# Performance work log

Hardware: AMD Instinct MI355X
Metric: run time of the kernel (lower is better)

The kernel has to match this reference:

```python
import jax, jax.numpy as jnp
import numpy as np

B, S, HID = 1, 2048, 4096
NH, NKV = 32, 8
HD = HID // NH          # 128
N_REP = NH // NKV       # 4
ROPE_THETA = 10000.0


def setup_inputs() -> dict:
    key = jax.random.key(0)
    ks = jax.random.split(key, 5)
    scale = 0.02
    x = jax.random.normal(ks[0], (B, S, HID), dtype=jnp.float32)
    Wq = jax.random.normal(ks[1], (HID, HID), dtype=jnp.float32) * scale
    Wk = jax.random.normal(ks[2], (NKV * HD, HID), dtype=jnp.float32) * scale
    Wv = jax.random.normal(ks[3], (NKV * HD, HID), dtype=jnp.float32) * scale
    Wo = jax.random.normal(ks[4], (HID, HID), dtype=jnp.float32) * scale
    position_ids = jnp.broadcast_to(jnp.arange(S, dtype=jnp.int32)[None, :], (B, S))
    return {"x": x, "Wq": Wq, "Wk": Wk, "Wv": Wv, "Wo": Wo, "position_ids": position_ids}


def _rope_cache(seq_len, dtype):
    inv_freq = 1.0 / (ROPE_THETA ** (jnp.arange(0, HD, 2, dtype=jnp.float32) / HD))
    t = jnp.arange(seq_len, dtype=jnp.float32)
    freqs = t[:, None] * inv_freq[None, :]            # [S, HD/2]
    emb = jnp.concatenate([freqs, freqs], axis=-1)    # [S, HD]
    return jnp.cos(emb).astype(dtype), jnp.sin(emb).astype(dtype)


def _rotate_half(x):
    x1, x2 = x[..., : HD // 2], x[..., HD // 2:]
    return jnp.concatenate([-x2, x1], axis=-1)


def reference(x, Wq, Wk, Wv, Wo, position_ids):
    b, s, _ = x.shape
    # projections (nn.Linear: x @ W.T)
    q = (x @ Wq.T).reshape(b, s, NH, HD).transpose(0, 2, 1, 3)    # [B,NH,S,HD]
    k = (x @ Wk.T).reshape(b, s, NKV, HD).transpose(0, 2, 1, 3)   # [B,NKV,S,HD]
    v = (x @ Wv.T).reshape(b, s, NKV, HD).transpose(0, 2, 1, 3)
    # RoPE
    cos_c, sin_c = _rope_cache(s, x.dtype)
    cos = cos_c[position_ids][:, None, :, :]   # [B,1,S,HD]
    sin = sin_c[position_ids][:, None, :, :]
    q = q * cos + _rotate_half(q) * sin
    k = k * cos + _rotate_half(k) * sin
    # GQA repeat_kv
    k = jnp.repeat(k, N_REP, axis=1)   # [B,NH,S,HD]
    v = jnp.repeat(v, N_REP, axis=1)
    # scaled dot-product attention with causal mask
    scores = jnp.einsum('bhqd,bhkd->bhqk', q, k) / jnp.sqrt(jnp.float32(HD))
    causal = jnp.tril(jnp.ones((s, s), dtype=bool))
    scores = jnp.where(causal[None, None, :, :], scores, jnp.finfo(scores.dtype).min)
    attn = jax.nn.softmax(scores.astype(jnp.float32), axis=-1).astype(q.dtype)
    out = jnp.einsum('bhqk,bhkd->bhqd', attn, v)                  # [B,NH,S,HD]
    out = out.transpose(0, 2, 1, 3).reshape(b, s, NH * HD)
    return out @ Wo.T
```

## Files before the change

kernel.cpp:

```cpp
#include <hip/hip_runtime.h>
#include <hip/hip_bf16.h>

#define DEVI __device__ __forceinline__

typedef __attribute__((ext_vector_type(8))) __bf16 bf16x8;
typedef __attribute__((ext_vector_type(4))) float f32x4;

DEVI f32x4 mfma_16x16x32(bf16x8 a, bf16x8 b, f32x4 c) {
  return __builtin_amdgcn_mfma_f32_16x16x32_bf16(a, b, c, 0, 0, 0);
}

DEVI void gld16(const void* g, void* l) {
  __builtin_amdgcn_global_load_lds(
      reinterpret_cast<const __attribute__((address_space(1))) unsigned int*>(
          reinterpret_cast<unsigned long long>(g)),
      reinterpret_cast<__attribute__((address_space(3))) unsigned int*>(
          reinterpret_cast<unsigned long long>(l)),
      16, 0, 0);
}

DEVI unsigned short f2bf(float f) {
  unsigned u = __builtin_bit_cast(unsigned, f);
  u += 0x7FFFu + ((u >> 16) & 1u);
  return (unsigned short)(u >> 16);
}
DEVI float bf2f(unsigned short b) {
  return __builtin_bit_cast(float, (unsigned)b << 16);
}

struct Conv5 {
  const float4 *x, *wq, *wk, *wv, *wo;
  ushort4 *xb, *wqb, *wkv, *wob;
};
__global__ void k_conv_all(Conv5 a) {
  constexpr int C0 = 2097152;
  constexpr int C1 = C0 + 4194304;
  constexpr int C2 = C1 + 1048576;
  constexpr int C3 = C2 + 1048576;
  constexpr int C4 = C3 + 4194304;
  int stride = gridDim.x * blockDim.x;
  for (int i = blockIdx.x * blockDim.x + threadIdx.x; i < C4; i += stride) {
    const float4* src; ushort4* dst; int j;
    if (i < C0)      { src = a.x;  dst = a.xb;            j = i; }
    else if (i < C1) { src = a.wq; dst = a.wqb;           j = i - C0; }
    else if (i < C2) { src = a.wk; dst = a.wkv;           j = i - C1; }
    else if (i < C3) { src = a.wv; dst = a.wkv + 1048576; j = i - C2; }
    else             { src = a.wo; dst = a.wob;           j = i - C3; }
    float4 v = src[j];
    ushort4 o; o.x = f2bf(v.x); o.y = f2bf(v.y); o.z = f2bf(v.z); o.w = f2bf(v.w);
    dst[j] = o;
  }
}

__global__ void k_rope_table(float2* __restrict__ tab) {
  int idx = blockIdx.x * blockDim.x + threadIdx.x;
  int s = idx >> 6, d = idx & 63;
  float invf = powf(10000.0f, -(float)d * (1.0f / 64.0f));
  float f = (float)s * invf;
  tab[idx] = make_float2(cosf(f), sinf(f));
}

template <int NH_, int L2NH>
__global__ void k_rope_v(unsigned short* __restrict__ X, const float2* __restrict__ tab,
                         const int* __restrict__ pos, float scale) {
  int t = blockIdx.x * blockDim.x + threadIdx.x;
  int d0 = (t & 7) * 8;
  int sh = t >> 3;
  int s  = sh >> L2NH;
  int h  = sh & (NH_ - 1);
  size_t base = (size_t)s * (NH_ * 128) + h * 128 + d0;
  const float4* tf = (const float4*)(tab + (size_t)pos[s] * 64 + d0);
  unsigned short a[8], b[8], oa[8], ob[8];
  *(ushort4*)&a[0] = *(const ushort4*)(X + base);
  *(ushort4*)&a[4] = *(const ushort4*)(X + base + 4);
  *(ushort4*)&b[0] = *(const ushort4*)(X + base + 64);
  *(ushort4*)&b[4] = *(const ushort4*)(X + base + 68);
#pragma unroll
  for (int j = 0; j < 4; ++j) {
    float4 cs = tf[j];
    float x1 = bf2f(a[2*j]),   x2 = bf2f(b[2*j]);
    float y1 = bf2f(a[2*j+1]), y2 = bf2f(b[2*j+1]);
    oa[2*j]   = f2bf((x1 * cs.x - x2 * cs.y) * scale);
    ob[2*j]   = f2bf((x2 * cs.x + x1 * cs.y) * scale);
    oa[2*j+1] = f2bf((y1 * cs.z - y2 * cs.w) * scale);
    ob[2*j+1] = f2bf((y2 * cs.z + y1 * cs.w) * scale);
  }
  *(ushort4*)(X + base)      = *(ushort4*)&oa[0];
  *(ushort4*)(X + base + 4)  = *(ushort4*)&oa[4];
  *(ushort4*)(X + base + 64) = *(ushort4*)&ob[0];
  *(ushort4*)(X + base + 68) = *(ushort4*)&ob[4];
}

template <int MODE>
__global__ __launch_bounds__(256, 2)
void k_gemm_bt(const unsigned short* __restrict__ A,
               const unsigned short* __restrict__ B,
               void* __restrict__ Cp, int M, int N, int K) {
  constexpr int BK = 32;
  __shared__ __align__(16) unsigned short As[128][BK];
  __shared__ __align__(16) unsigned short Bs[128][BK];
  const int tid  = threadIdx.x;
  const int lane = tid & 63;
  const int wave = tid >> 6;
  const int bm = blockIdx.y * 128;
  const int bn = blockIdx.x * 128;
  const int wm = (wave >> 1) * 64;
  const int wn = (wave & 1) * 64;
  const int l15 = lane & 15;
  const int lg  = lane >> 4;

  f32x4 acc[4][4] = {};

  const int srow = lane >> 2;
  const int scol = (lane & 3) * 8;
  const unsigned short* aS0 = A + (size_t)(bm + wave * 32 + srow) * K + scol;
  const unsigned short* aS1 = aS0 + (size_t)16 * K;
  const unsigned short* bS0 = B + (size_t)(bn + wave * 32 + srow) * K + scol;
  const unsigned short* bS1 = bS0 + (size_t)16 * K;

  for (int k0 = 0; k0 < K; k0 += BK) {
    __syncthreads();
    gld16(aS0 + k0, &As[wave * 32][0]);
    gld16(aS1 + k0, &As[wave * 32 + 16][0]);
    gld16(bS0 + k0, &Bs[wave * 32][0]);
    gld16(bS1 + k0, &Bs[wave * 32 + 16][0]);
    __syncthreads();

    bf16x8 a[4], b[4];
#pragma unroll
    for (int m = 0; m < 4; ++m) a[m] = *(const bf16x8*)&As[wm + m * 16 + l15][lg * 8];
#pragma unroll
    for (int n = 0; n < 4; ++n) b[n] = *(const bf16x8*)&Bs[wn + n * 16 + l15][lg * 8];
#pragma unroll
    for (int m = 0; m < 4; ++m)
#pragma unroll
      for (int n = 0; n < 4; ++n)
        acc[m][n] = mfma_16x16x32(a[m], b[n], acc[m][n]);
  }

#pragma unroll
  for (int m = 0; m < 4; ++m)
#pragma unroll
    for (int n = 0; n < 4; ++n)
#pragma unroll
      for (int r = 0; r < 4; ++r) {
        int row = bm + wm + m * 16 + lg * 4 + r;
        int col = bn + wn + n * 16 + l15;
        float v = acc[m][n][r];
        if (MODE == 0) ((unsigned short*)Cp)[(size_t)row * N + col] = f2bf(v);
        else           ((float*)Cp)[(size_t)row * N + col] = v;
      }
}

__global__ __launch_bounds__(256, 2)
void k_gemm_kv(const unsigned short* __restrict__ A,
               const unsigned short* __restrict__ B,
               unsigned short* __restrict__ Kp,
               unsigned short* __restrict__ Vtp,
               int M, int K) {
  constexpr int BK = 32;
  __shared__ __align__(16) unsigned short As[64][BK];
  __shared__ __align__(16) unsigned short Bs[128][BK];
  const int tid = threadIdx.x, lane = tid & 63, wave = tid >> 6;
  const int bm = blockIdx.y * 64;
  const int bn = blockIdx.x * 128;
  const int wn = wave * 32;
  const int l15 = lane & 15, lg = lane >> 4;
  f32x4 acc[4][2] = {};
  const int srow = lane >> 2, scol = (lane & 3) * 8;
  const unsigned short* aS0 = A + (size_t)(bm + wave * 16 + srow) * K + scol;
  const unsigned short* bS0 = B + (size_t)(bn + wave * 32 + srow) * K + scol;
  const unsigned short* bS1 = bS0 + (size_t)16 * K;

  for (int k0 = 0; k0 < K; k0 += BK) {
    __syncthreads();
    gld16(aS0 + k0, &As[wave * 16][0]);
    gld16(bS0 + k0, &Bs[wave * 32][0]);
    gld16(bS1 + k0, &Bs[wave * 32 + 16][0]);
    __syncthreads();
    bf16x8 a[4], b[2];
#pragma unroll
    for (int m = 0; m < 4; ++m) a[m] = *(const bf16x8*)&As[m * 16 + l15][lg * 8];
#pragma unroll
    for (int n = 0; n < 2; ++n) b[n] = *(const bf16x8*)&Bs[wn + n * 16 + l15][lg * 8];
#pragma unroll
    for (int m = 0; m < 4; ++m)
#pragma unroll
      for (int n = 0; n < 2; ++n)
        acc[m][n] = mfma_16x16x32(a[m], b[n], acc[m][n]);
  }

#pragma unroll
  for (int m = 0; m < 4; ++m)
#pragma unroll
    for (int n = 0; n < 2; ++n)
#pragma unroll
      for (int r = 0; r < 4; ++r) {
        int row = bm + m * 16 + lg * 4 + r;
        int col = bn + wn + n * 16 + l15;
        float v = acc[m][n][r];
        if (col < 1024) Kp[(size_t)row * 1024 + col] = f2bf(v);
        else            Vtp[(size_t)(col - 1024) * 2048 + row] = f2bf(v);
      }
}

__global__ __launch_bounds__(256, 2)
void k_attn(const unsigned short* __restrict__ Q,
            const unsigned short* __restrict__ Kb,
            const unsigned short* __restrict__ Vt,
            unsigned short* __restrict__ AO) {
  __shared__ __align__(16) unsigned short Kl[2][64][128];
  __shared__ __align__(16) unsigned short Vl[2][128][64];
  __shared__ __align__(16) unsigned short Pl[4][16][72];
  const int tid = threadIdx.x, lane = tid & 63, w = tid >> 6;
  const int bid = blockIdx.x;
  const int qi = 31 - (bid >> 5);
  const int h  = bid & 31;
  const int q0 = qi * 64;
  const int kh = h >> 2;
  const int l15 = lane & 15, lg = lane >> 4;

  bf16x8 qf[4];
  {
    const unsigned short* qr = Q + (size_t)(q0 + w * 16 + l15) * 4096 + h * 128;
#pragma unroll
    for (int ks = 0; ks < 4; ++ks) qf[ks] = *(const bf16x8*)(qr + ks * 32 + lg * 8);
  }

  f32x4 o[8] = {};
  float m_run = -1e30f, l_run = 0.f;
  const int nkb = qi + 1;
  const int myq = q0 + w * 16 + l15;

  auto stageK = [&](int buf, int kv0) {
#pragma unroll
    for (int c = 0; c < 4; ++c) {
      int row = 16 * w + 4 * c + lg;
      gld16(Kb + (size_t)(kv0 + row) * 1024 + kh * 128 + ((l15 ^ (row & 7)) * 8),
            &Kl[buf][16 * w + 4 * c][0]);
    }
  };
  auto stageV = [&](int buf, int kv0) {
#pragma unroll
    for (int c = 0; c < 4; ++c) {
      int row = 32 * w + 8 * c + (lane >> 3);
      gld16(Vt + (size_t)(kh * 128 + row) * 2048 + kv0 + (((lane & 7) ^ (row & 7)) * 8),
            &Vl[buf][32 * w + 8 * c][0]);
    }
  };

  stageK(0, 0);
  stageV(0, 0);
  int cur = 0;

  for (int kb = 0; kb < nkb; ++kb) {
    const int kv0 = kb * 64;
    __syncthreads();
    if (kb + 1 < nkb) { stageK(cur ^ 1, kv0 + 64); stageV(cur ^ 1, kv0 + 64); }

    f32x4 s[4] = {};
    __builtin_amdgcn_s_setprio(1);
#pragma unroll
    for (int ks = 0; ks < 4; ++ks)
#pragma unroll
      for (int n = 0; n < 4; ++n) {
        bf16x8 bk = *(const bf16x8*)&Kl[cur][n * 16 + l15][((ks * 4 + lg) ^ (l15 & 7)) * 8];
        s[n] = mfma_16x16x32(bk, qf[ks], s[n]);
      }
    __builtin_amdgcn_s_setprio(0);

    if (kb == nkb - 1) {
#pragma unroll
      for (int n = 0; n < 4; ++n)
#pragma unroll
        for (int r = 0; r < 4; ++r)
          if (kv0 + n * 16 + lg * 4 + r > myq) s[n][r] = -1e30f;
    }

    float mx = -1e30f;
#pragma unroll
    for (int n = 0; n < 4; ++n)
      mx = fmaxf(mx, fmaxf(fmaxf(s[n][0], s[n][1]), fmaxf(s[n][2], s[n][3])));
    mx = fmaxf(mx, __shfl_xor(mx, 16));
    mx = fmaxf(mx, __shfl_xor(mx, 32));
    float mn = fmaxf(m_run, mx);
    float fac = __expf(m_run - mn);
    m_run = mn;
    float rs = 0.f;
#pragma unroll
    for (int n = 0; n < 4; ++n)
#pragma unroll
      for (int r = 0; r < 4; ++r) {
        float pv = __expf(s[n][r] - mn);
        s[n][r] = pv;
        rs += pv;
      }
    rs += __shfl_xor(rs, 16);
    rs += __shfl_xor(rs, 32);
    l_run = l_run * fac + rs;
#pragma unroll
    for (int j = 0; j < 8; ++j) {
      o[j][0] *= fac; o[j][1] *= fac; o[j][2] *= fac; o[j][3] *= fac;
    }

#pragma unroll
    for (int n = 0; n < 4; ++n)
#pragma unroll
      for (int r = 0; r < 4; ++r)
        Pl[w][l15][n * 16 + lg * 4 + r] = f2bf(s[n][r]);
    asm volatile("s_waitcnt lgkmcnt(0)" ::: "memory");
    bf16x8 pa0 = *(const bf16x8*)&Pl[w][l15][lg * 8];
    bf16x8 pa1 = *(const bf16x8*)&Pl[w][l15][32 + lg * 8];

    __builtin_amdgcn_s_setprio(1);
#pragma unroll
    for (int j = 0; j < 8; ++j) {
      bf16x8 bv0 = *(const bf16x8*)&Vl[cur][j * 16 + l15][(lg ^ (l15 & 7)) * 8];
      bf16x8 bv1 = *(const bf16x8*)&Vl[cur][j * 16 + l15][((4 + lg) ^ (l15 & 7)) * 8];
      o[j] = mfma_16x16x32(bv0, pa0, o[j]);
      o[j] = mfma_16x16x32(bv1, pa1, o[j]);
    }
    __builtin_amdgcn_s_setprio(0);
    cur ^= 1;
  }

  float inv = 1.0f / l_run;
  __syncthreads();
  unsigned short* Ol = &Kl[0][0][0];
#pragma unroll
  for (int j = 0; j < 8; ++j)
#pragma unroll
    for (int r = 0; r < 4; ++r)
      Ol[w * 2176 + l15 * 136 + j * 16 + lg * 4 + r] = f2bf(o[j][r] * inv);
  asm volatile("s_waitcnt lgkmcnt(0)" ::: "memory");
#pragma unroll
  for (int p = 0; p < 4; ++p) {
    int row = p * 4 + lg;
    bf16x8 vv = *(const bf16x8*)&Ol[w * 2176 + row * 136 + l15 * 8];
    *(bf16x8*)(AO + (size_t)(q0 + w * 16 + row) * 4096 + h * 128 + l15 * 8) = vv;
  }
}

extern "C" void kernel_launch(void* const* d_in, const int* in_sizes, int n_in,
                              void* d_out, int out_size, void* d_ws, size_t ws_size,
                              hipStream_t stream) {
  const float* x  = (const float*)d_in[0];
  const float* Wq = (const float*)d_in[1];
  const float* Wk = (const float*)d_in[2];
  const float* Wv = (const float*)d_in[3];
  const float* Wo = (const float*)d_in[4];
  const int*   pos = (const int*)d_in[5];
  float* out = (float*)d_out;

  char* p = (char*)d_ws;
  unsigned short* xb  = (unsigned short*)p; p += (size_t)2048 * 4096 * 2;
  unsigned short* wqb = (unsigned short*)p; p += (size_t)4096 * 4096 * 2;
  unsigned short* wkv = (unsigned short*)p; p += (size_t)2048 * 4096 * 2;
  unsigned short* wob = (unsigned short*)p; p += (size_t)4096 * 4096 * 2;
  unsigned short* qb  = (unsigned short*)p; p += (size_t)2048 * 4096 * 2;
  unsigned short* kb  = (unsigned short*)p; p += (size_t)2048 * 1024 * 2;
  unsigned short* vtb = (unsigned short*)p; p += (size_t)1024 * 2048 * 2;
  unsigned short* aob = (unsigned short*)p; p += (size_t)2048 * 4096 * 2;
  float2*         tab = (float2*)p;         p += (size_t)2048 * 64 * 8;

  Conv5 ca;
  ca.x  = (const float4*)x;  ca.wq = (const float4*)Wq; ca.wk = (const float4*)Wk;
  ca.wv = (const float4*)Wv; ca.wo = (const float4*)Wo;
  ca.xb = (ushort4*)xb; ca.wqb = (ushort4*)wqb; ca.wkv = (ushort4*)wkv; ca.wob = (ushort4*)wob;
  k_conv_all<<<4096, 256, 0, stream>>>(ca);
  k_rope_table<<<512, 256, 0, stream>>>(tab);

  k_gemm_bt<0><<<dim3(32, 16), 256, 0, stream>>>(xb, wqb, qb, 2048, 4096, 4096);
  k_gemm_kv<<<dim3(16, 32), 256, 0, stream>>>(xb, wkv, kb, vtb, 2048, 4096);

  const float scale = 0.08838834764831845f;
  k_rope_v<32, 5><<<2048, 256, 0, stream>>>(qb, tab, pos, scale);
  k_rope_v<8, 3><<<512, 256, 0, stream>>>(kb, tab, pos, 1.0f);

  k_attn<<<1024, 256, 0, stream>>>(qb, kb, vtb, aob);

  k_gemm_bt<1><<<dim3(32, 16), 256, 0, stream>>>(aob, wob, out, 2048, 4096, 4096);
}
```

Before: 560.1 us.

## Fuse QKV projections into one GEMM, widen K tile with swizzle, lazy softmax rescale

Packs Wq, Wk and Wv into one contiguous bf16 weight buffer so a single GEMM launch with 48 column tiles produces Q, K and transposed V, and routes each column in the epilogue. The GEMM now loads 64-wide K tiles with an XOR-swizzled LDS layout, halving barrier rounds per K and reducing bank conflicts. The attention kernel skips the running-max rescale unless some row's max grows by more than 8, saving exp and multiplies at some risk to range, and writes P to LDS as packed 4-element stores. LDS per block doubles, which may affect occupancy.

```diff
diff --git a/kernel.cpp b/kernel.cpp
--- a/kernel.cpp
+++ b/kernel.cpp
@@ -30,7 +30,7 @@
 
 struct Conv5 {
   const float4 *x, *wq, *wk, *wv, *wo;
-  ushort4 *xb, *wqb, *wkv, *wob;
+  ushort4 *xb, *wqkv, *wob;
 };
 __global__ void k_conv_all(Conv5 a) {
   constexpr int C0 = 2097152;
@@ -41,11 +41,11 @@
   int stride = gridDim.x * blockDim.x;
   for (int i = blockIdx.x * blockDim.x + threadIdx.x; i < C4; i += stride) {
     const float4* src; ushort4* dst; int j;
-    if (i < C0)      { src = a.x;  dst = a.xb;            j = i; }
-    else if (i < C1) { src = a.wq; dst = a.wqb;           j = i - C0; }
-    else if (i < C2) { src = a.wk; dst = a.wkv;           j = i - C1; }
-    else if (i < C3) { src = a.wv; dst = a.wkv + 1048576; j = i - C2; }
-    else             { src = a.wo; dst = a.wob;           j = i - C3; }
+    if (i < C0)      { src = a.x;  dst = a.xb;             j = i; }
+    else if (i < C1) { src = a.wq; dst = a.wqkv;           j = i - C0; }
+    else if (i < C2) { src = a.wk; dst = a.wqkv + 4194304; j = i - C1; }
+    else if (i < C3) { src = a.wv; dst = a.wqkv + 5242880; j = i - C2; }
+    else             { src = a.wo; dst = a.wob;            j = i - C3; }
     float4 v = src[j];
     ushort4 o; o.x = f2bf(v.x); o.y = f2bf(v.y); o.z = f2bf(v.z); o.w = f2bf(v.w);
     dst[j] = o;
@@ -91,14 +91,16 @@
   *(ushort4*)(X + base + 68) = *(ushort4*)&ob[4];
 }
 
-template <int MODE>
+template <int EPI>
 __global__ __launch_bounds__(256, 2)
-void k_gemm_bt(const unsigned short* __restrict__ A,
-               const unsigned short* __restrict__ B,
-               void* __restrict__ Cp, int M, int N, int K) {
-  constexpr int BK = 32;
-  __shared__ __align__(16) unsigned short As[128][BK];
-  __shared__ __align__(16) unsigned short Bs[128][BK];
+void k_gemm64(const unsigned short* __restrict__ A,
+              const unsigned short* __restrict__ B,
+              void* __restrict__ Cp,
+              unsigned short* __restrict__ Kp,
+              unsigned short* __restrict__ Vtp,
+              int K) {
+  __shared__ __align__(16) unsigned short As[128][64];
+  __shared__ __align__(16) unsigned short Bs[128][64];
   const int tid  = threadIdx.x;
   const int lane = tid & 63;
   const int wave = tid >> 6;
@@ -111,31 +113,35 @@
 
   f32x4 acc[4][4] = {};
 
-  const int srow = lane >> 2;
-  const int scol = (lane & 3) * 8;
-  const unsigned short* aS0 = A + (size_t)(bm + wave * 32 + srow) * K + scol;
-  const unsigned short* aS1 = aS0 + (size_t)16 * K;
-  const unsigned short* bS0 = B + (size_t)(bn + wave * 32 + srow) * K + scol;
-  const unsigned short* bS1 = bS0 + (size_t)16 * K;
-
-  for (int k0 = 0; k0 < K; k0 += BK) {
+  const int srow  = lane >> 3;
+  const int scol  = ((lane & 7) ^ srow) * 8;
+  const unsigned short* aS = A + (size_t)(bm + wave * 32 + srow) * K + scol;
+  const unsigned short* bS = B + (size_t)(bn + wave * 32 + srow) * K + scol;
+
+  for (int k0 = 0; k0 < K; k0 += 64) {
     __syncthreads();
-    gld16(aS0 + k0, &As[wave * 32][0]);
-    gld16(aS1 + k0, &As[wave * 32 + 16][0]);
-    gld16(bS0 + k0, &Bs[wave * 32][0]);
-    gld16(bS1 + k0, &Bs[wave * 32 + 16][0]);
+#pragma unroll
+    for (int c = 0; c < 4; ++c) {
+      gld16(aS + (size_t)(c * 8) * K + k0, &As[wave * 32 + c * 8][0]);
+      gld16(bS + (size_t)(c * 8) * K + k0, &Bs[wave * 32 + c * 8][0]);
+    }
     __syncthreads();
 
-    bf16x8 a[4], b[4];
-#pragma unroll
-    for (int m = 0; m < 4; ++m) a[m] = *(const bf16x8*)&As[wm + m * 16 + l15][lg * 8];
-#pragma unroll
-    for (int n = 0; n < 4; ++n) b[n] = *(const bf16x8*)&Bs[wn + n * 16 + l15][lg * 8];
-#pragma unroll
-    for (int m = 0; m < 4; ++m)
+#pragma unroll
+    for (int ks = 0; ks < 2; ++ks) {
+      bf16x8 a[4], b[4];
+#pragma unroll
+      for (int m = 0; m < 4; ++m)
+        a[m] = *(const bf16x8*)&As[wm + m * 16 + l15][((ks * 4 + lg) ^ (l15 & 7)) * 8];
 #pragma unroll
       for (int n = 0; n < 4; ++n)
-        acc[m][n] = mfma_16x16x32(a[m], b[n], acc[m][n]);
+        b[n] = *(const bf16x8*)&Bs[wn + n * 16 + l15][((ks * 4 + lg) ^ (l15 & 7)) * 8];
+#pragma unroll
+      for (int m = 0; m < 4; ++m)
+#pragma unroll
+        for (int n = 0; n < 4; ++n)
+          acc[m][n] = mfma_16x16x32(a[m], b[n], acc[m][n]);
+    }
   }
 
 #pragma unroll
@@ -147,60 +153,13 @@
         int row = bm + wm + m * 16 + lg * 4 + r;
         int col = bn + wn + n * 16 + l15;
         float v = acc[m][n][r];
-        if (MODE == 0) ((unsigned short*)Cp)[(size_t)row * N + col] = f2bf(v);
-        else           ((float*)Cp)[(size_t)row * N + col] = v;
-      }
-}
-
-__global__ __launch_bounds__(256, 2)
-void k_gemm_kv(const unsigned short* __restrict__ A,
-               const unsigned short* __restrict__ B,
-               unsigned short* __restrict__ Kp,
-               unsigned short* __restrict__ Vtp,
-               int M, int K) {
-  constexpr int BK = 32;
-  __shared__ __align__(16) unsigned short As[64][BK];
-  __shared__ __align__(16) unsigned short Bs[128][BK];
-  const int tid = threadIdx.x, lane = tid & 63, wave = tid >> 6;
-  const int bm = blockIdx.y * 64;
-  const int bn = blockIdx.x * 128;
-  const int wn = wave * 32;
-  const int l15 = lane & 15, lg = lane >> 4;
-  f32x4 acc[4][2] = {};
-  const int srow = lane >> 2, scol = (lane & 3) * 8;
-  const unsigned short* aS0 = A + (size_t)(bm + wave * 16 + srow) * K + scol;
-  const unsigned short* bS0 = B + (size_t)(bn + wave * 32 + srow) * K + scol;
-  const unsigned short* bS1 = bS0 + (size_t)16 * K;
-
-  for (int k0 = 0; k0 < K; k0 += BK) {
-    __syncthreads();
-    gld16(aS0 + k0, &As[wave * 16][0]);
-    gld16(bS0 + k0, &Bs[wave * 32][0]);
-    gld16(bS1 + k0, &Bs[wave * 32 + 16][0]);
-    __syncthreads();
-    bf16x8 a[4], b[2];
-#pragma unroll
-    for (int m = 0; m < 4; ++m) a[m] = *(const bf16x8*)&As[m * 16 + l15][lg * 8];
-#pragma unroll
-    for (int n = 0; n < 2; ++n) b[n] = *(const bf16x8*)&Bs[wn + n * 16 + l15][lg * 8];
-#pragma unroll
-    for (int m = 0; m < 4; ++m)
-#pragma unroll
-      for (int n = 0; n < 2; ++n)
-        acc[m][n] = mfma_16x16x32(a[m], b[n], acc[m][n]);
-  }
-
-#pragma unroll
-  for (int m = 0; m < 4; ++m)
-#pragma unroll
-    for (int n = 0; n < 2; ++n)
-#pragma unroll
-      for (int r = 0; r < 4; ++r) {
-        int row = bm + m * 16 + lg * 4 + r;
-        int col = bn + wn + n * 16 + l15;
-        float v = acc[m][n][r];
-        if (col < 1024) Kp[(size_t)row * 1024 + col] = f2bf(v);
-        else            Vtp[(size_t)(col - 1024) * 2048 + row] = f2bf(v);
+        if (EPI == 0) {
+          if (col < 4096)      ((unsigned short*)Cp)[(size_t)row * 4096 + col] = f2bf(v);
+          else if (col < 5120) Kp[(size_t)row * 1024 + (col - 4096)] = f2bf(v);
+          else                 Vtp[(size_t)(col - 5120) * 2048 + row] = f2bf(v);
+        } else {
+          ((float*)Cp)[(size_t)row * 4096 + col] = v;
+        }
       }
 }
 
@@ -283,31 +242,36 @@
       mx = fmaxf(mx, fmaxf(fmaxf(s[n][0], s[n][1]), fmaxf(s[n][2], s[n][3])));
     mx = fmaxf(mx, __shfl_xor(mx, 16));
     mx = fmaxf(mx, __shfl_xor(mx, 32));
-    float mn = fmaxf(m_run, mx);
-    float fac = __expf(m_run - mn);
-    m_run = mn;
+
+    if (!__all(mx <= m_run + 8.0f)) {
+      float mn = fmaxf(m_run, mx);
+      float fac = __expf(m_run - mn);
+      m_run = mn;
+      l_run *= fac;
+#pragma unroll
+      for (int j = 0; j < 8; ++j) {
+        o[j][0] *= fac; o[j][1] *= fac; o[j][2] *= fac; o[j][3] *= fac;
+      }
+    }
     float rs = 0.f;
 #pragma unroll
     for (int n = 0; n < 4; ++n)
 #pragma unroll
       for (int r = 0; r < 4; ++r) {
-        float pv = __expf(s[n][r] - mn);
+        float pv = __expf(s[n][r] - m_run);
         s[n][r] = pv;
         rs += pv;
       }
     rs += __shfl_xor(rs, 16);
     rs += __shfl_xor(rs, 32);
-    l_run = l_run * fac + rs;
-#pragma unroll
-    for (int j = 0; j < 8; ++j) {
-      o[j][0] *= fac; o[j][1] *= fac; o[j][2] *= fac; o[j][3] *= fac;
-    }
-
-#pragma unroll
-    for (int n = 0; n < 4; ++n)
-#pragma unroll
-      for (int r = 0; r < 4; ++r)
-        Pl[w][l15][n * 16 + lg * 4 + r] = f2bf(s[n][r]);
+    l_run += rs;
+
+#pragma unroll
+    for (int n = 0; n < 4; ++n) {
+      ushort4 pk;
+      pk.x = f2bf(s[n][0]); pk.y = f2bf(s[n][1]); pk.z = f2bf(s[n][2]); pk.w = f2bf(s[n][3]);
+      *(ushort4*)&Pl[w][l15][n * 16 + lg * 4] = pk;
+    }
     asm volatile("s_waitcnt lgkmcnt(0)" ::: "memory");
     bf16x8 pa0 = *(const bf16x8*)&Pl[w][l15][lg * 8];
     bf16x8 pa1 = *(const bf16x8*)&Pl[w][l15][32 + lg * 8];
@@ -353,25 +317,23 @@
   float* out = (float*)d_out;
 
   char* p = (char*)d_ws;
-  unsigned short* xb  = (unsigned short*)p; p += (size_t)2048 * 4096 * 2;
-  unsigned short* wqb = (unsigned short*)p; p += (size_t)4096 * 4096 * 2;
-  unsigned short* wkv = (unsigned short*)p; p += (size_t)2048 * 4096 * 2;
-  unsigned short* wob = (unsigned short*)p; p += (size_t)4096 * 4096 * 2;
-  unsigned short* qb  = (unsigned short*)p; p += (size_t)2048 * 4096 * 2;
-  unsigned short* kb  = (unsigned short*)p; p += (size_t)2048 * 1024 * 2;
-  unsigned short* vtb = (unsigned short*)p; p += (size_t)1024 * 2048 * 2;
-  unsigned short* aob = (unsigned short*)p; p += (size_t)2048 * 4096 * 2;
-  float2*         tab = (float2*)p;         p += (size_t)2048 * 64 * 8;
+  unsigned short* xb   = (unsigned short*)p; p += (size_t)2048 * 4096 * 2;
+  unsigned short* wqkv = (unsigned short*)p; p += (size_t)6144 * 4096 * 2;
+  unsigned short* wob  = (unsigned short*)p; p += (size_t)4096 * 4096 * 2;
+  unsigned short* qb   = (unsigned short*)p; p += (size_t)2048 * 4096 * 2;
+  unsigned short* kb   = (unsigned short*)p; p += (size_t)2048 * 1024 * 2;
+  unsigned short* vtb  = (unsigned short*)p; p += (size_t)1024 * 2048 * 2;
+  unsigned short* aob  = (unsigned short*)p; p += (size_t)2048 * 4096 * 2;
+  float2*         tab  = (float2*)p;         p += (size_t)2048 * 64 * 8;
 
   Conv5 ca;
   ca.x  = (const float4*)x;  ca.wq = (const float4*)Wq; ca.wk = (const float4*)Wk;
   ca.wv = (const float4*)Wv; ca.wo = (const float4*)Wo;
-  ca.xb = (ushort4*)xb; ca.wqb = (ushort4*)wqb; ca.wkv = (ushort4*)wkv; ca.wob = (ushort4*)wob;
+  ca.xb = (ushort4*)xb; ca.wqkv = (ushort4*)wqkv; ca.wob = (ushort4*)wob;
   k_conv_all<<<4096, 256, 0, stream>>>(ca);
   k_rope_table<<<512, 256, 0, stream>>>(tab);
 
-  k_gemm_bt<0><<<dim3(32, 16), 256, 0, stream>>>(xb, wqb, qb, 2048, 4096, 4096);
-  k_gemm_kv<<<dim3(16, 32), 256, 0, stream>>>(xb, wkv, kb, vtb, 2048, 4096);
+  k_gemm64<0><<<dim3(48, 16), 256, 0, stream>>>(xb, wqkv, qb, kb, vtb, 4096);
 
   const float scale = 0.08838834764831845f;
   k_rope_v<32, 5><<<2048, 256, 0, stream>>>(qb, tab, pos, scale);
@@ -379,5 +341,5 @@
 
   k_attn<<<1024, 256, 0, stream>>>(qb, kb, vtb, aob);
 
-  k_gemm_bt<1><<<dim3(32, 16), 256, 0, stream>>>(aob, wob, out, 2048, 4096, 4096);
-}
+  k_gemm64<1><<<dim3(32, 16), 256, 0, stream>>>(aob, wob, out, nullptr, nullptr, 4096);
+}
```

Result: faster. 479.7 us (-14.3%).
